# Performance work log

Measured on AMD Instinct MI355X. Metric: run time of the kernel, lower is better.

The kernel has to match this reference:

```python
import jax, jax.numpy as jnp
import numpy as np

N_EMBD = 768
N_HEAD = 12
HEAD_SIZE = 64  # n_embd // n_head
LN_EPS = 1e-5


def layer_norm(x, g, b):
    mu = jnp.mean(x, axis=-1, keepdims=True)
    var = jnp.var(x, axis=-1, keepdims=True)
    return (x - mu) * jax.lax.rsqrt(var + LN_EPS) * g + b


def setup_inputs() -> dict:
    key = jax.random.key(0)
    ks = jax.random.split(key, 12)
    B, T, C, H, D = 4, 2048, N_EMBD, N_HEAD, HEAD_SIZE
    s = 0.02
    return {
        "x": jax.random.normal(ks[0], (B, T, C), jnp.float32),
        "wq": jax.random.normal(ks[1], (H, C, D), jnp.float32) * s,
        "wk": jax.random.normal(ks[2], (H, C, D), jnp.float32) * s,
        "wv": jax.random.normal(ks[3], (H, C, D), jnp.float32) * s,
        "w_proj": jax.random.normal(ks[4], (C, C), jnp.float32) * s,
        "b_proj": jnp.zeros((C,), jnp.float32),
        "w1": jax.random.normal(ks[5], (C, 4 * C), jnp.float32) * s,
        "b1": jnp.zeros((4 * C,), jnp.float32),
        "w2": jax.random.normal(ks[6], (4 * C, C), jnp.float32) * s,
        "b2": jnp.zeros((C,), jnp.float32),
        "ln1_g": jnp.ones((C,), jnp.float32),
        "ln1_b": jnp.zeros((C,), jnp.float32),
        "ln2_g": jnp.ones((C,), jnp.float32),
        "ln2_b": jnp.zeros((C,), jnp.float32),
    }


def reference(x, wq, wk, wv, w_proj, b_proj, w1, b1, w2, b2,
              ln1_g, ln1_b, ln2_g, ln2_b):
    B, T, C = x.shape
    # --- self-attention sublayer (dropout in eval mode -> identity) ---
    h = layer_norm(x, ln1_g, ln1_b)
    q = jnp.einsum('btc,hcd->bhtd', h, wq)
    k = jnp.einsum('btc,hcd->bhtd', h, wk)
    v = jnp.einsum('btc,hcd->bhtd', h, wv)
    scores = jnp.einsum('bhtd,bhsd->bhts', q, k) * (HEAD_SIZE ** -0.5)
    causal = jnp.tril(jnp.ones((T, T), bool))
    scores = jnp.where(causal, scores, -jnp.inf)
    attn = jax.nn.softmax(scores, axis=-1)  # [B,H,T,T]
    out = jnp.einsum('bhts,bhsd->bhtd', attn, v)
    out = out.transpose(0, 2, 1, 3).reshape(B, T, C)  # concat heads
    x = x + out @ w_proj + b_proj
    # --- FFN sublayer ---
    h2 = layer_norm(x, ln2_g, ln2_b)
    x = x + jax.nn.relu(h2 @ w1 + b1) @ w2 + b2
    return x
```

## Files before the change

kernel.cpp:

```cpp
#include <hip/hip_runtime.h>
#include <hip/hip_bf16.h>

typedef __attribute__((ext_vector_type(8))) short bf16x8;
typedef __attribute__((ext_vector_type(4))) short bf16x4;
typedef __attribute__((ext_vector_type(4))) float f32x4;

#define AS1 __attribute__((address_space(1)))
#define AS3 __attribute__((address_space(3)))

__global__ __launch_bounds__(256)
void ln_kernel(const float* __restrict__ x, const float* __restrict__ g,
               const float* __restrict__ b, __hip_bfloat16* __restrict__ out)
{
    const int row = blockIdx.x;
    const float* xr = x + (size_t)row * 768;
    const int t = threadIdx.x;
    float v0 = xr[t], v1 = xr[t + 256], v2 = xr[t + 512];
    float s = v0 + v1 + v2;
    float ss = v0 * v0 + v1 * v1 + v2 * v2;
#pragma unroll
    for (int off = 1; off < 64; off <<= 1) {
        s  += __shfl_xor(s, off, 64);
        ss += __shfl_xor(ss, off, 64);
    }
    __shared__ float red[8];
    const int wv = t >> 6;
    if ((t & 63) == 0) { red[wv] = s; red[wv + 4] = ss; }
    __syncthreads();
    s  = red[0] + red[1] + red[2] + red[3];
    ss = red[4] + red[5] + red[6] + red[7];
    const float mu = s * (1.0f / 768.0f);
    const float rstd = rsqrtf(ss * (1.0f / 768.0f) - mu * mu + 1e-5f);
    __hip_bfloat16* orow = out + (size_t)row * 768;
    orow[t]       = __float2bfloat16((v0 - mu) * rstd * g[t]       + b[t]);
    orow[t + 256] = __float2bfloat16((v1 - mu) * rstd * g[t + 256] + b[t + 256]);
    orow[t + 512] = __float2bfloat16((v2 - mu) * rstd * g[t + 512] + b[t + 512]);
}

__global__ __launch_bounds__(256)
void transpose_w(const float* __restrict__ in, __hip_bfloat16* __restrict__ out,
                 int R, int C)
{
    __shared__ float tile[32][33];
    const int c0 = blockIdx.x * 32, r0 = blockIdx.y * 32;
    const int tx = threadIdx.x, ty = threadIdx.y;
#pragma unroll
    for (int i = 0; i < 4; i++)
        tile[ty + i * 8][tx] = in[(size_t)(r0 + ty + i * 8) * C + c0 + tx];
    __syncthreads();
#pragma unroll
    for (int i = 0; i < 4; i++)
        out[(size_t)(c0 + ty + i * 8) * R + r0 + tx] =
            __float2bfloat16(tile[tx][ty + i * 8]);
}

__global__ __launch_bounds__(256)
void conv_qkv(const float* __restrict__ wq, const float* __restrict__ wk,
              const float* __restrict__ wv, __hip_bfloat16* __restrict__ out)
{
    const int z = blockIdx.z;
    const int mat = z / 12, h = z % 12;
    const float* w = (mat == 0) ? wq : ((mat == 1) ? wk : wv);
    __shared__ float tile[32][33];
    const int c0 = blockIdx.x * 32;
    const int d0 = blockIdx.y * 32;
    const int tx = threadIdx.x, ty = threadIdx.y;
#pragma unroll
    for (int i = 0; i < 4; i++)
        tile[ty + i * 8][tx] =
            w[(size_t)h * 768 * 64 + (size_t)(c0 + ty + i * 8) * 64 + d0 + tx];
    __syncthreads();
#pragma unroll
    for (int i = 0; i < 4; i++)
        out[(size_t)(mat * 768 + h * 64 + d0 + ty + i * 8) * 768 + c0 + tx] =
            __float2bfloat16(tile[tx][ty + i * 8]);
}

template<int MODE>
__global__ __launch_bounds__(256)
void gemm_kernel(const __hip_bfloat16* __restrict__ A,
                 const __hip_bfloat16* __restrict__ Bt,
                 const float* __restrict__ bias,
                 const float* __restrict__ res,
                 void* __restrict__ outp,
                 __hip_bfloat16* __restrict__ outK,
                 __hip_bfloat16* __restrict__ outV,
                 int M, int N, int K)
{
    __shared__ alignas(16) char As[128 * 128];
    __shared__ alignas(16) char Bs[128 * 128];
    const int tid = threadIdx.x;
    const int wave = tid >> 6, lane = tid & 63;

    const int nwgx = gridDim.x;
    const int hw = blockIdx.x + nwgx * blockIdx.y;
    const int nwg = nwgx * gridDim.y;
    const int q8 = nwg >> 3;
    const int work = (hw & 7) * q8 + (hw >> 3);
    const int m0 = (work / nwgx) * 128, n0 = (work % nwgx) * 128;

    const int wm = (wave >> 1) * 64, wn = (wave & 1) * 64;
    f32x4 acc[4][4] = {};

    int soff[4];
#pragma unroll
    for (int r = 0; r < 4; r++) {
        const int n = tid + 256 * r;
        const int row = n >> 3;
        soff[r] = row * (K * 2) + ((((n & 7) << 4)) ^ ((row & 7) << 4));
    }

    const int fr = lane & 15, fg = lane >> 4;

    for (int k0 = 0; k0 < K; k0 += 64) {
        __syncthreads();
        const char* ga = (const char*)A  + (size_t)m0 * K * 2 + k0 * 2;
        const char* gb = (const char*)Bt + (size_t)n0 * K * 2 + k0 * 2;
#pragma unroll
        for (int r = 0; r < 4; r++) {
            __builtin_amdgcn_global_load_lds((const AS1 void*)(ga + soff[r]),
                (AS3 void*)(As + r * 4096 + tid * 16), 16, 0, 0);
            __builtin_amdgcn_global_load_lds((const AS1 void*)(gb + soff[r]),
                (AS3 void*)(Bs + r * 4096 + tid * 16), 16, 0, 0);
        }
        __syncthreads();
        bf16x8 af[4][2], bfr[4][2];
#pragma unroll
        for (int i = 0; i < 4; i++)
#pragma unroll
            for (int ks = 0; ks < 2; ks++)
                af[i][ks] = *(const bf16x8*)(As + (wm + i * 16 + fr) * 128 +
                            ((fg * 16 + ks * 64) ^ ((fr & 7) << 4)));
#pragma unroll
        for (int j = 0; j < 4; j++)
#pragma unroll
            for (int ks = 0; ks < 2; ks++)
                bfr[j][ks] = *(const bf16x8*)(Bs + (wn + j * 16 + fr) * 128 +
                             ((fg * 16 + ks * 64) ^ ((fr & 7) << 4)));
        __builtin_amdgcn_s_setprio(1);
#pragma unroll
        for (int ks = 0; ks < 2; ks++)
#pragma unroll
            for (int i = 0; i < 4; i++)
#pragma unroll
                for (int j = 0; j < 4; j++)
                    acc[i][j] = __builtin_amdgcn_mfma_f32_16x16x32_bf16(
                        af[i][ks], bfr[j][ks], acc[i][j], 0, 0, 0);
        __builtin_amdgcn_s_setprio(0);
    }

#pragma unroll
    for (int j = 0; j < 4; j++) {
        const int n = n0 + wn + j * 16 + fr;
        if (MODE == 1 && n >= 1536) {
            const int hh = (n - 1536) >> 6, dd = (n - 1536) & 63;
#pragma unroll
            for (int i = 0; i < 4; i++) {
                const int m = m0 + wm + i * 16 + fg * 4;
                const int bidx = m >> 11, tt = m & 2047;
                bf16x4 pk;
                __hip_bfloat16* pp = (__hip_bfloat16*)&pk;
#pragma unroll
                for (int r = 0; r < 4; r++)
                    pp[r] = __float2bfloat16(acc[i][j][r]);
                *(bf16x4*)&outV[(((size_t)bidx * 12 + hh) * 64 + dd) * 2048 + tt] = pk;
            }
            continue;
        }
        const float bv = (MODE == 2 || MODE == 3) ? bias[n] : 0.0f;
#pragma unroll
        for (int i = 0; i < 4; i++) {
#pragma unroll
            for (int r = 0; r < 4; r++) {
                const int m = m0 + wm + i * 16 + fg * 4 + r;
                float v = acc[i][j][r] + bv;
                if (MODE == 3) v = fmaxf(v, 0.0f);
                if (MODE == 2) {
                    ((float*)outp)[(size_t)m * N + n] = res[(size_t)m * N + n] + v;
                } else if (MODE == 1) {
                    __hip_bfloat16* dst; int nc;
                    if (n < 768) { dst = (__hip_bfloat16*)outp; nc = n;
                                   v *= 0.18033688011112042f;  }
                    else         { dst = outK; nc = n - 768; }
                    const int hh = nc >> 6, dd = nc & 63;
                    const int bidx = m >> 11, tt = m & 2047;
                    dst[(((size_t)bidx * 12 + hh) * 2048 + tt) * 64 + dd] =
                        __float2bfloat16(v);
                } else {
                    ((__hip_bfloat16*)outp)[(size_t)m * N + n] = __float2bfloat16(v);
                }
            }
        }
    }
}

__global__ __launch_bounds__(256)
void attn_kernel(const __hip_bfloat16* __restrict__ Q,
                 const __hip_bfloat16* __restrict__ Kg,
                 const __hip_bfloat16* __restrict__ Vg,
                 __hip_bfloat16* __restrict__ out)
{
    __shared__ alignas(16) char lds[32768];
    const int tid = threadIdx.x, wave = tid >> 6, lane = tid & 63;
    const int fr = lane & 15, fg = lane >> 4;

    const int hw = blockIdx.x + 16 * blockIdx.y;
    const int xcd = hw & 7, chunk = hw >> 3;
    const int bh = xcd * 6 + (chunk >> 4);
    const int bx = chunk & 15;

    const int b = bh / 12, h = bh % 12;
    const __hip_bfloat16* qb = Q  + (size_t)bh * 2048 * 64;
    const __hip_bfloat16* kb = Kg + (size_t)bh * 2048 * 64;
    const __hip_bfloat16* vb = Vg + (size_t)bh * 2048 * 64;

    int ksoff[2], vsoff[2];
#pragma unroll
    for (int r = 0; r < 2; r++) {
        const int n = wave * 64 + lane + 256 * r;
        const int row = n >> 3;
        const int swz = (((n & 7) << 4)) ^ ((row & 7) << 4);
        ksoff[r] = row * 128  + swz;
        vsoff[r] = row * 4096 + swz;
    }

    auto STAGE = [&](int cur, int kv0) {
        const char* kx = (const char*)kb + (size_t)kv0 * 128;
        const char* vx = (const char*)vb + (size_t)kv0 * 2;
#pragma unroll
        for (int r = 0; r < 2; r++) {
            __builtin_amdgcn_global_load_lds((const AS1 void*)(kx + ksoff[r]),
                (AS3 void*)(lds + cur * 16384 + r * 4096 + wave * 1024), 16, 0, 0);
            __builtin_amdgcn_global_load_lds((const AS1 void*)(vx + vsoff[r]),
                (AS3 void*)(lds + cur * 16384 + 8192 + r * 4096 + wave * 1024), 16, 0, 0);
        }
    };

    const bf16x4 ones = {(short)0x3F80, (short)0x3F80,
                         (short)0x3F80, (short)0x3F80};

#pragma unroll
    for (int pass = 0; pass < 2; ++pass) {
        const int g = pass ? (31 - bx) : bx;
        const int q0w = g * 64 + wave * 16;
        const int qv = q0w + fr;

        bf16x8 qf0 = *(const bf16x8*)(qb + (size_t)qv * 64 + fg * 8);
        bf16x8 qf1 = *(const bf16x8*)(qb + (size_t)qv * 64 + 32 + fg * 8);

        f32x4 o[4] = {};
        f32x4 o_l = {};
        float mrun = -1e30f;
        const int NT = g + 1;

        STAGE(0, 0);
        __syncthreads();
        int cur = 0;

        for (int t = 0; t < NT; ++t) {
            if (t + 1 < NT) STAGE(cur ^ 1, (t + 1) << 6);
            const int kv0 = t << 6;
            const char* Kb = lds + cur * 16384;
            const char* Vb = Kb + 8192;
            bf16x8 kf[4][2];
#pragma unroll
            for (int c = 0; c < 4; c++)
#pragma unroll
                for (int hh = 0; hh < 2; hh++)
                    kf[c][hh] = *(const bf16x8*)(Kb + (16 * c + fr) * 128 +
                                ((hh * 64 + fg * 16) ^ ((fr & 7) << 4)));
            f32x4 s[4];
            __builtin_amdgcn_s_setprio(1);
#pragma unroll
            for (int c = 0; c < 4; c++) {
                f32x4 z = {};
                s[c] = __builtin_amdgcn_mfma_f32_16x16x32_bf16(
                    kf[c][0], qf0, z, 0, 0, 0);
                s[c] = __builtin_amdgcn_mfma_f32_16x16x32_bf16(
                    kf[c][1], qf1, s[c], 0, 0, 0);
            }
            __builtin_amdgcn_s_setprio(0);
            if (t == NT - 1) {
#pragma unroll
                for (int c = 0; c < 4; c++)
#pragma unroll
                    for (int r = 0; r < 4; r++)
                        if (kv0 + 16 * c + 4 * fg + r > qv) s[c][r] = -1e30f;
            }
            float t0 = fmaxf(fmaxf(s[0][0], s[0][1]), fmaxf(s[0][2], s[0][3]));
            float t1 = fmaxf(fmaxf(s[1][0], s[1][1]), fmaxf(s[1][2], s[1][3]));
            float t2 = fmaxf(fmaxf(s[2][0], s[2][1]), fmaxf(s[2][2], s[2][3]));
            float t3 = fmaxf(fmaxf(s[3][0], s[3][1]), fmaxf(s[3][2], s[3][3]));
            const float tm = fmaxf(fmaxf(t0, t1), fmaxf(t2, t3));
            if (!__all(tm <= mrun + 8.f)) {
                float tf = fmaxf(tm, __shfl_xor(tm, 16, 64));
                tf = fmaxf(tf, __shfl_xor(tf, 32, 64));
                const float mnew = fmaxf(mrun, tf);
                const float al = exp2f(mrun - mnew);
#pragma unroll
                for (int i = 0; i < 4; i++)
#pragma unroll
                    for (int e = 0; e < 4; e++) o[i][e] *= al;
#pragma unroll
                for (int e = 0; e < 4; e++) o_l[e] *= al;
                mrun = mnew;
            }
            bf16x4 pf[4];
#pragma unroll
            for (int c = 0; c < 4; c++) {
                const float p0 = exp2f(s[c][0] - mrun), p1 = exp2f(s[c][1] - mrun);
                const float p2 = exp2f(s[c][2] - mrun), p3 = exp2f(s[c][3] - mrun);
                __hip_bfloat16* pp = (__hip_bfloat16*)&pf[c];
                pp[0] = __float2bfloat16(p0); pp[1] = __float2bfloat16(p1);
                pp[2] = __float2bfloat16(p2); pp[3] = __float2bfloat16(p3);
            }
            bf16x4 vf[4][4];
#pragma unroll
            for (int i = 0; i < 4; i++)
#pragma unroll
                for (int c = 0; c < 4; c++)
                    vf[i][c] = *(const bf16x4*)(Vb + (16 * i + fr) * 128 +
                                ((32 * c + 8 * fg) ^ ((fr & 7) << 4)));
            __builtin_amdgcn_s_setprio(1);
#pragma unroll
            for (int c = 0; c < 4; c++)
                o_l = __builtin_amdgcn_mfma_f32_16x16x16bf16_1k(
                    ones, pf[c], o_l, 0, 0, 0);
#pragma unroll
            for (int i = 0; i < 4; i++)
#pragma unroll
                for (int c = 0; c < 4; c++)
                    o[i] = __builtin_amdgcn_mfma_f32_16x16x16bf16_1k(
                        vf[i][c], pf[c], o[i], 0, 0, 0);
            __builtin_amdgcn_s_setprio(0);
            __syncthreads();
            cur ^= 1;
        }

        const float inv = 1.0f / o_l[0];
        __hip_bfloat16* ob = out + ((size_t)(b * 2048 + qv)) * 768 + h * 64;
#pragma unroll
        for (int i = 0; i < 4; i++) {
            bf16x4 pk;
            __hip_bfloat16* pp = (__hip_bfloat16*)&pk;
#pragma unroll
            for (int r = 0; r < 4; r++)
                pp[r] = __float2bfloat16(o[i][r] * inv);
            *(bf16x4*)(ob + 16 * i + 4 * fg) = pk;
        }
    }
}

extern "C" void kernel_launch(void* const* d_in, const int* in_sizes, int n_in,
                              void* d_out, int out_size, void* d_ws, size_t ws_size,
                              hipStream_t stream)
{
    const float* x      = (const float*)d_in[0];
    const float* wq     = (const float*)d_in[1];
    const float* wk     = (const float*)d_in[2];
    const float* wv     = (const float*)d_in[3];
    const float* w_proj = (const float*)d_in[4];
    const float* b_proj = (const float*)d_in[5];
    const float* w1     = (const float*)d_in[6];
    const float* b1     = (const float*)d_in[7];
    const float* w2     = (const float*)d_in[8];
    const float* b2     = (const float*)d_in[9];
    const float* ln1_g  = (const float*)d_in[10];
    const float* ln1_b  = (const float*)d_in[11];
    const float* ln2_g  = (const float*)d_in[12];
    const float* ln2_b  = (const float*)d_in[13];
    float* out = (float*)d_out;

    char* w = (char*)d_ws;
    size_t off = 0;
    auto alloc = [&](size_t bytes) {
        void* p = w + off;
        off += (bytes + 255) & ~(size_t)255;
        return p;
    };
    __hip_bfloat16* h_ln    = (__hip_bfloat16*)alloc(8192ull * 768 * 2);
    __hip_bfloat16* wt_qkv  = (__hip_bfloat16*)alloc(2304ull * 768 * 2);
    __hip_bfloat16* wt_proj = (__hip_bfloat16*)alloc(768ull * 768 * 2);
    __hip_bfloat16* wt1     = (__hip_bfloat16*)alloc(3072ull * 768 * 2);
    __hip_bfloat16* wt2     = (__hip_bfloat16*)alloc(768ull * 3072 * 2);
    __hip_bfloat16* qbuf    = (__hip_bfloat16*)alloc(8192ull * 768 * 2);
    __hip_bfloat16* kbuf    = (__hip_bfloat16*)alloc(8192ull * 768 * 2);
    __hip_bfloat16* vbuf    = (__hip_bfloat16*)alloc(8192ull * 768 * 2);
    __hip_bfloat16* attn_o  = (__hip_bfloat16*)alloc(8192ull * 768 * 2);
    float*          x1      = (float*)alloc(8192ull * 768 * 4);
    __hip_bfloat16* h2      = (__hip_bfloat16*)alloc(8192ull * 768 * 2);
    __hip_bfloat16* a1      = qbuf;

    conv_qkv<<<dim3(24, 2, 36), dim3(32, 8), 0, stream>>>(wq, wk, wv, wt_qkv);
    transpose_w<<<dim3(24, 24), dim3(32, 8), 0, stream>>>(w_proj, wt_proj, 768, 768);
    transpose_w<<<dim3(96, 24), dim3(32, 8), 0, stream>>>(w1, wt1, 768, 3072);
    transpose_w<<<dim3(24, 96), dim3(32, 8), 0, stream>>>(w2, wt2, 3072, 768);

    ln_kernel<<<8192, 256, 0, stream>>>(x, ln1_g, ln1_b, h_ln);
    gemm_kernel<1><<<dim3(18, 64), 256, 0, stream>>>(
        h_ln, wt_qkv, nullptr, nullptr, qbuf, kbuf, vbuf, 8192, 2304, 768);
    attn_kernel<<<dim3(16, 48), 256, 0, stream>>>(qbuf, kbuf, vbuf, attn_o);
    gemm_kernel<2><<<dim3(6, 64), 256, 0, stream>>>(
        attn_o, wt_proj, b_proj, x, x1, nullptr, nullptr, 8192, 768, 768);

    ln_kernel<<<8192, 256, 0, stream>>>(x1, ln2_g, ln2_b, h2);
    gemm_kernel<3><<<dim3(24, 64), 256, 0, stream>>>(
        h2, wt1, b1, nullptr, a1, nullptr, nullptr, 8192, 3072, 768);
    gemm_kernel<2><<<dim3(6, 64), 256, 0, stream>>>(
        a1, wt2, b2, x1, out, nullptr, nullptr, 8192, 768, 3072);
}
```

Measured before the change: 249.6 us.

## Add 128x64 GEMM tile variant and fold running max into score MFMA accumulator

Templates the GEMM on tile width and uses 128x64 tiles (four waves stacked along M) for the QKV, projection and FFN-down GEMMs. This doubles the workgroup count for the narrow-N GEMMs to fill more CUs, but lowers data reuse per tile. In attention, the negated running max is now passed as the initial accumulator of the QK^T MFMA. This removes the per-element max subtraction before exp2, at the cost of rescaling the scores and accumulator when the max grows.

```diff
diff --git a/kernel.cpp b/kernel.cpp
--- a/kernel.cpp
+++ b/kernel.cpp
@@ -76,7 +76,7 @@
             __float2bfloat16(tile[tx][ty + i * 8]);
 }
 
-template<int MODE>
+template<int MODE, int BN>
 __global__ __launch_bounds__(256)
 void gemm_kernel(const __hip_bfloat16* __restrict__ A,
                  const __hip_bfloat16* __restrict__ Bt,
@@ -87,8 +87,10 @@
                  __hip_bfloat16* __restrict__ outV,
                  int M, int N, int K)
 {
+    constexpr int MREP = (BN == 128) ? 4 : 2;
+    constexpr int BCH  = BN / 32;
     __shared__ alignas(16) char As[128 * 128];
-    __shared__ alignas(16) char Bs[128 * 128];
+    __shared__ alignas(16) char Bs[BN * 128];
     const int tid = threadIdx.x;
     const int wave = tid >> 6, lane = tid & 63;
 
@@ -97,10 +99,11 @@
     const int nwg = nwgx * gridDim.y;
     const int q8 = nwg >> 3;
     const int work = (hw & 7) * q8 + (hw >> 3);
-    const int m0 = (work / nwgx) * 128, n0 = (work % nwgx) * 128;
-
-    const int wm = (wave >> 1) * 64, wn = (wave & 1) * 64;
-    f32x4 acc[4][4] = {};
+    const int m0 = (work / nwgx) * 128, n0 = (work % nwgx) * BN;
+
+    const int wm = (BN == 128) ? (wave >> 1) * 64 : wave * 32;
+    const int wn = (BN == 128) ? (wave & 1) * 64 : 0;
+    f32x4 acc[MREP][4] = {};
 
     int soff[4];
 #pragma unroll
@@ -117,16 +120,17 @@
         const char* ga = (const char*)A  + (size_t)m0 * K * 2 + k0 * 2;
         const char* gb = (const char*)Bt + (size_t)n0 * K * 2 + k0 * 2;
 #pragma unroll
-        for (int r = 0; r < 4; r++) {
+        for (int r = 0; r < 4; r++)
             __builtin_amdgcn_global_load_lds((const AS1 void*)(ga + soff[r]),
                 (AS3 void*)(As + r * 4096 + tid * 16), 16, 0, 0);
+#pragma unroll
+        for (int r = 0; r < BCH; r++)
             __builtin_amdgcn_global_load_lds((const AS1 void*)(gb + soff[r]),
                 (AS3 void*)(Bs + r * 4096 + tid * 16), 16, 0, 0);
-        }
         __syncthreads();
-        bf16x8 af[4][2], bfr[4][2];
-#pragma unroll
-        for (int i = 0; i < 4; i++)
+        bf16x8 af[MREP][2], bfr[4][2];
+#pragma unroll
+        for (int i = 0; i < MREP; i++)
 #pragma unroll
             for (int ks = 0; ks < 2; ks++)
                 af[i][ks] = *(const bf16x8*)(As + (wm + i * 16 + fr) * 128 +
@@ -141,7 +145,7 @@
 #pragma unroll
         for (int ks = 0; ks < 2; ks++)
 #pragma unroll
-            for (int i = 0; i < 4; i++)
+            for (int i = 0; i < MREP; i++)
 #pragma unroll
                 for (int j = 0; j < 4; j++)
                     acc[i][j] = __builtin_amdgcn_mfma_f32_16x16x32_bf16(
@@ -155,7 +159,7 @@
         if (MODE == 1 && n >= 1536) {
             const int hh = (n - 1536) >> 6, dd = (n - 1536) & 63;
 #pragma unroll
-            for (int i = 0; i < 4; i++) {
+            for (int i = 0; i < MREP; i++) {
                 const int m = m0 + wm + i * 16 + fg * 4;
                 const int bidx = m >> 11, tt = m & 2047;
                 bf16x4 pk;
@@ -169,7 +173,7 @@
         }
         const float bv = (MODE == 2 || MODE == 3) ? bias[n] : 0.0f;
 #pragma unroll
-        for (int i = 0; i < 4; i++) {
+        for (int i = 0; i < MREP; i++) {
 #pragma unroll
             for (int r = 0; r < 4; r++) {
                 const int m = m0 + wm + i * 16 + fg * 4 + r;
@@ -250,7 +254,7 @@
 
         f32x4 o[4] = {};
         f32x4 o_l = {};
-        float mrun = -1e30f;
+        f32x4 nm4 = {1e4f, 1e4f, 1e4f, 1e4f};
         const int NT = g + 1;
 
         STAGE(0, 0);
@@ -273,9 +277,8 @@
             __builtin_amdgcn_s_setprio(1);
 #pragma unroll
             for (int c = 0; c < 4; c++) {
-                f32x4 z = {};
                 s[c] = __builtin_amdgcn_mfma_f32_16x16x32_bf16(
-                    kf[c][0], qf0, z, 0, 0, 0);
+                    kf[c][0], qf0, nm4, 0, 0, 0);
                 s[c] = __builtin_amdgcn_mfma_f32_16x16x32_bf16(
                     kf[c][1], qf1, s[c], 0, 0, 0);
             }
@@ -287,29 +290,34 @@
                     for (int r = 0; r < 4; r++)
                         if (kv0 + 16 * c + 4 * fg + r > qv) s[c][r] = -1e30f;
             }
-            float t0 = fmaxf(fmaxf(s[0][0], s[0][1]), fmaxf(s[0][2], s[0][3]));
-            float t1 = fmaxf(fmaxf(s[1][0], s[1][1]), fmaxf(s[1][2], s[1][3]));
-            float t2 = fmaxf(fmaxf(s[2][0], s[2][1]), fmaxf(s[2][2], s[2][3]));
-            float t3 = fmaxf(fmaxf(s[3][0], s[3][1]), fmaxf(s[3][2], s[3][3]));
-            const float tm = fmaxf(fmaxf(t0, t1), fmaxf(t2, t3));
-            if (!__all(tm <= mrun + 8.f)) {
+            const float a0 = fmaxf(fmaxf(s[0][0], s[0][1]), s[0][2]);
+            const float a1 = fmaxf(fmaxf(s[0][3], s[1][0]), s[1][1]);
+            const float a2 = fmaxf(fmaxf(s[1][2], s[1][3]), s[2][0]);
+            const float a3 = fmaxf(fmaxf(s[2][1], s[2][2]), s[2][3]);
+            const float a4 = fmaxf(fmaxf(s[3][0], s[3][1]), s[3][2]);
+            const float b0 = fmaxf(fmaxf(a0, a1), a2);
+            const float b1 = fmaxf(fmaxf(a3, a4), s[3][3]);
+            const float tm = fmaxf(b0, b1);
+            if (!__all(tm <= 8.f)) {
                 float tf = fmaxf(tm, __shfl_xor(tm, 16, 64));
                 tf = fmaxf(tf, __shfl_xor(tf, 32, 64));
-                const float mnew = fmaxf(mrun, tf);
-                const float al = exp2f(mrun - mnew);
+                const float al = exp2f(-tf);
+#pragma unroll
+                for (int c = 0; c < 4; c++)
+#pragma unroll
+                    for (int r = 0; r < 4; r++) s[c][r] -= tf;
 #pragma unroll
                 for (int i = 0; i < 4; i++)
 #pragma unroll
                     for (int e = 0; e < 4; e++) o[i][e] *= al;
 #pragma unroll
-                for (int e = 0; e < 4; e++) o_l[e] *= al;
-                mrun = mnew;
+                for (int e = 0; e < 4; e++) { o_l[e] *= al; nm4[e] -= tf; }
             }
             bf16x4 pf[4];
 #pragma unroll
             for (int c = 0; c < 4; c++) {
-                const float p0 = exp2f(s[c][0] - mrun), p1 = exp2f(s[c][1] - mrun);
-                const float p2 = exp2f(s[c][2] - mrun), p3 = exp2f(s[c][3] - mrun);
+                const float p0 = exp2f(s[c][0]), p1 = exp2f(s[c][1]);
+                const float p2 = exp2f(s[c][2]), p3 = exp2f(s[c][3]);
                 __hip_bfloat16* pp = (__hip_bfloat16*)&pf[c];
                 pp[0] = __float2bfloat16(p0); pp[1] = __float2bfloat16(p1);
                 pp[2] = __float2bfloat16(p2); pp[3] = __float2bfloat16(p3);
@@ -397,15 +405,15 @@
     transpose_w<<<dim3(24, 96), dim3(32, 8), 0, stream>>>(w2, wt2, 3072, 768);
 
     ln_kernel<<<8192, 256, 0, stream>>>(x, ln1_g, ln1_b, h_ln);
-    gemm_kernel<1><<<dim3(18, 64), 256, 0, stream>>>(
+    gemm_kernel<1, 64><<<dim3(36, 64), 256, 0, stream>>>(
         h_ln, wt_qkv, nullptr, nullptr, qbuf, kbuf, vbuf, 8192, 2304, 768);
     attn_kernel<<<dim3(16, 48), 256, 0, stream>>>(qbuf, kbuf, vbuf, attn_o);
-    gemm_kernel<2><<<dim3(6, 64), 256, 0, stream>>>(
+    gemm_kernel<2, 64><<<dim3(12, 64), 256, 0, stream>>>(
         attn_o, wt_proj, b_proj, x, x1, nullptr, nullptr, 8192, 768, 768);
 
     ln_kernel<<<8192, 256, 0, stream>>>(x1, ln2_g, ln2_b, h2);
-    gemm_kernel<3><<<dim3(24, 64), 256, 0, stream>>>(
+    gemm_kernel<3, 128><<<dim3(24, 64), 256, 0, stream>>>(
         h2, wt1, b1, nullptr, a1, nullptr, nullptr, 8192, 3072, 768);
-    gemm_kernel<2><<<dim3(6, 64), 256, 0, stream>>>(
+    gemm_kernel<2, 64><<<dim3(12, 64), 256, 0, stream>>>(
         a1, wt2, b2, x1, out, nullptr, nullptr, 8192, 768, 3072);
 }
```

Result: slower. 255.0 us (+2.2%).

## Double attention KV tile to 128 keys per iteration with 64KB LDS

Applied to the files above, without the earlier changes.

The causal attention kernel now stages and processes 128 keys per loop iteration instead of 64. The LDS double buffer grows to 64KB, and the global-to-LDS staging offsets and V swizzle are reworked for the wider tile. K and V fragment loads now sit next to their MFMAs instead of being hoisted. This halves the number of iterations, barriers and online-softmax rescale checks. In exchange it cuts workgroups per CU because of the larger LDS footprint, and wastes compute on a fully masked half-tile for some query blocks.

```diff
diff --git a/kernel.cpp b/kernel.cpp
--- a/kernel.cpp
+++ b/kernel.cpp
@@ -200,7 +200,7 @@
                  const __hip_bfloat16* __restrict__ Vg,
                  __hip_bfloat16* __restrict__ out)
 {
-    __shared__ alignas(16) char lds[32768];
+    __shared__ alignas(16) char lds[65536];
     const int tid = threadIdx.x, wave = tid >> 6, lane = tid & 63;
     const int fr = lane & 15, fg = lane >> 4;
 
@@ -214,25 +214,25 @@
     const __hip_bfloat16* kb = Kg + (size_t)bh * 2048 * 64;
     const __hip_bfloat16* vb = Vg + (size_t)bh * 2048 * 64;
 
-    int ksoff[2], vsoff[2];
-#pragma unroll
-    for (int r = 0; r < 2; r++) {
-        const int n = wave * 64 + lane + 256 * r;
-        const int row = n >> 3;
-        const int swz = (((n & 7) << 4)) ^ ((row & 7) << 4);
-        ksoff[r] = row * 128  + swz;
-        vsoff[r] = row * 4096 + swz;
+    int ksoff[4], vsoff[4];
+#pragma unroll
+    for (int r = 0; r < 4; r++) {
+        const int n = tid + 256 * r;
+        const int krow = n >> 3;
+        ksoff[r] = krow * 128 + ((((n & 7) << 4)) ^ ((krow & 7) << 4));
+        const int vrow = n >> 4;
+        vsoff[r] = vrow * 4096 + ((((n & 15) << 4)) ^ ((vrow & 7) << 4));
     }
 
     auto STAGE = [&](int cur, int kv0) {
         const char* kx = (const char*)kb + (size_t)kv0 * 128;
         const char* vx = (const char*)vb + (size_t)kv0 * 2;
 #pragma unroll
-        for (int r = 0; r < 2; r++) {
+        for (int r = 0; r < 4; r++) {
             __builtin_amdgcn_global_load_lds((const AS1 void*)(kx + ksoff[r]),
-                (AS3 void*)(lds + cur * 16384 + r * 4096 + wave * 1024), 16, 0, 0);
+                (AS3 void*)(lds + cur * 32768 + r * 4096 + tid * 16), 16, 0, 0);
             __builtin_amdgcn_global_load_lds((const AS1 void*)(vx + vsoff[r]),
-                (AS3 void*)(lds + cur * 16384 + 8192 + r * 4096 + wave * 1024), 16, 0, 0);
+                (AS3 void*)(lds + cur * 32768 + 16384 + r * 4096 + tid * 16), 16, 0, 0);
         }
     };
 
@@ -251,47 +251,43 @@
         f32x4 o[4] = {};
         f32x4 o_l = {};
         float mrun = -1e30f;
-        const int NT = g + 1;
+        const int NT = (g >> 1) + 1;
 
         STAGE(0, 0);
         __syncthreads();
         int cur = 0;
 
         for (int t = 0; t < NT; ++t) {
-            if (t + 1 < NT) STAGE(cur ^ 1, (t + 1) << 6);
-            const int kv0 = t << 6;
-            const char* Kb = lds + cur * 16384;
-            const char* Vb = Kb + 8192;
-            bf16x8 kf[4][2];
-#pragma unroll
-            for (int c = 0; c < 4; c++)
-#pragma unroll
-                for (int hh = 0; hh < 2; hh++)
-                    kf[c][hh] = *(const bf16x8*)(Kb + (16 * c + fr) * 128 +
-                                ((hh * 64 + fg * 16) ^ ((fr & 7) << 4)));
-            f32x4 s[4];
+            if (t + 1 < NT) STAGE(cur ^ 1, (t + 1) << 7);
+            const int kv0 = t << 7;
+            const char* Kb = lds + cur * 32768;
+            const char* Vb = Kb + 16384;
+            f32x4 s[8];
             __builtin_amdgcn_s_setprio(1);
 #pragma unroll
-            for (int c = 0; c < 4; c++) {
+            for (int c = 0; c < 8; c++) {
+                const bf16x8 kf0 = *(const bf16x8*)(Kb + (16 * c + fr) * 128 +
+                                   ((fg * 16) ^ ((fr & 7) << 4)));
+                const bf16x8 kf1 = *(const bf16x8*)(Kb + (16 * c + fr) * 128 +
+                                   ((64 + fg * 16) ^ ((fr & 7) << 4)));
                 f32x4 z = {};
-                s[c] = __builtin_amdgcn_mfma_f32_16x16x32_bf16(
-                    kf[c][0], qf0, z, 0, 0, 0);
-                s[c] = __builtin_amdgcn_mfma_f32_16x16x32_bf16(
-                    kf[c][1], qf1, s[c], 0, 0, 0);
+                s[c] = __builtin_amdgcn_mfma_f32_16x16x32_bf16(kf0, qf0, z, 0, 0, 0);
+                s[c] = __builtin_amdgcn_mfma_f32_16x16x32_bf16(kf1, qf1, s[c], 0, 0, 0);
             }
             __builtin_amdgcn_s_setprio(0);
             if (t == NT - 1) {
 #pragma unroll
-                for (int c = 0; c < 4; c++)
+                for (int c = 0; c < 8; c++)
 #pragma unroll
                     for (int r = 0; r < 4; r++)
                         if (kv0 + 16 * c + 4 * fg + r > qv) s[c][r] = -1e30f;
             }
-            float t0 = fmaxf(fmaxf(s[0][0], s[0][1]), fmaxf(s[0][2], s[0][3]));
-            float t1 = fmaxf(fmaxf(s[1][0], s[1][1]), fmaxf(s[1][2], s[1][3]));
-            float t2 = fmaxf(fmaxf(s[2][0], s[2][1]), fmaxf(s[2][2], s[2][3]));
-            float t3 = fmaxf(fmaxf(s[3][0], s[3][1]), fmaxf(s[3][2], s[3][3]));
-            const float tm = fmaxf(fmaxf(t0, t1), fmaxf(t2, t3));
+            float pm[8];
+#pragma unroll
+            for (int c = 0; c < 8; c++)
+                pm[c] = fmaxf(fmaxf(s[c][0], s[c][1]), fmaxf(s[c][2], s[c][3]));
+            float tm = fmaxf(fmaxf(fmaxf(pm[0], pm[1]), fmaxf(pm[2], pm[3])),
+                             fmaxf(fmaxf(pm[4], pm[5]), fmaxf(pm[6], pm[7])));
             if (!__all(tm <= mrun + 8.f)) {
                 float tf = fmaxf(tm, __shfl_xor(tm, 16, 64));
                 tf = fmaxf(tf, __shfl_xor(tf, 32, 64));
@@ -305,33 +301,28 @@
                 for (int e = 0; e < 4; e++) o_l[e] *= al;
                 mrun = mnew;
             }
-            bf16x4 pf[4];
-#pragma unroll
-            for (int c = 0; c < 4; c++) {
+            bf16x4 pf[8];
+#pragma unroll
+            for (int c = 0; c < 8; c++) {
                 const float p0 = exp2f(s[c][0] - mrun), p1 = exp2f(s[c][1] - mrun);
                 const float p2 = exp2f(s[c][2] - mrun), p3 = exp2f(s[c][3] - mrun);
                 __hip_bfloat16* pp = (__hip_bfloat16*)&pf[c];
                 pp[0] = __float2bfloat16(p0); pp[1] = __float2bfloat16(p1);
                 pp[2] = __float2bfloat16(p2); pp[3] = __float2bfloat16(p3);
             }
-            bf16x4 vf[4][4];
-#pragma unroll
-            for (int i = 0; i < 4; i++)
-#pragma unroll
-                for (int c = 0; c < 4; c++)
-                    vf[i][c] = *(const bf16x4*)(Vb + (16 * i + fr) * 128 +
-                                ((32 * c + 8 * fg) ^ ((fr & 7) << 4)));
             __builtin_amdgcn_s_setprio(1);
 #pragma unroll
-            for (int c = 0; c < 4; c++)
+            for (int c = 0; c < 8; c++) {
                 o_l = __builtin_amdgcn_mfma_f32_16x16x16bf16_1k(
                     ones, pf[c], o_l, 0, 0, 0);
 #pragma unroll
-            for (int i = 0; i < 4; i++)
-#pragma unroll
-                for (int c = 0; c < 4; c++)
+                for (int i = 0; i < 4; i++) {
+                    const bf16x4 vf = *(const bf16x4*)(Vb + (16 * i + fr) * 256 +
+                                      ((32 * c + 8 * fg) ^ ((fr & 7) << 4)));
                     o[i] = __builtin_amdgcn_mfma_f32_16x16x16bf16_1k(
-                        vf[i][c], pf[c], o[i], 0, 0, 0);
+                        vf, pf[c], o[i], 0, 0, 0);
+                }
+            }
             __builtin_amdgcn_s_setprio(0);
             __syncthreads();
             cur ^= 1;
```

Result: slower. 261.1 us (+4.6%).
